# Kernel tuning notes

Measured on AMD Instinct MI355X. Metric: run time of the kernel, lower is better.

The kernel has to match this reference:

```python
import jax, jax.numpy as jnp
import numpy as np
from jax import lax

NUM_HEADS = 8
DIM = 384
B, H, W = 4, 128, 128
NEG_INF = -1e30


def setup_inputs() -> dict:
    key = jax.random.key(0)
    ks = jax.random.split(key, 5)
    x = jax.random.normal(ks[0], (B, DIM, H, W), dtype=jnp.float32)
    qkv_w = jax.random.normal(ks[1], (3 * DIM, DIM), dtype=jnp.float32) * 0.02   # 1x1 conv weight
    dw_w = jax.random.normal(ks[2], (3 * DIM, 1, 3, 3), dtype=jnp.float32) * 0.02  # depthwise 3x3
    proj_w = jax.random.normal(ks[3], (DIM, DIM), dtype=jnp.float32) * 0.02     # 1x1 conv weight
    temperature = jnp.ones((NUM_HEADS, 1, 1), dtype=jnp.float32)
    a1 = jnp.array([0.2], dtype=jnp.float32)
    a2 = jnp.array([0.2], dtype=jnp.float32)
    a3 = jnp.array([0.2], dtype=jnp.float32)
    a4 = jnp.array([0.2], dtype=jnp.float32)
    return {"x": x, "qkv_w": qkv_w, "dw_w": dw_w, "proj_w": proj_w,
            "temperature": temperature, "a1": a1, "a2": a2, "a3": a3, "a4": a4}


def _topk_softmax(attn, k):
    # keep top-k along last dim, softmax over kept entries (threshold == k-th largest)
    thr = lax.top_k(attn, k)[0][..., -1:]
    return jax.nn.softmax(jnp.where(attn >= thr, attn, NEG_INF), axis=-1)


def reference(x, qkv_w, dw_w, proj_w, temperature, a1, a2, a3, a4):
    b, c, h, w = x.shape
    head = NUM_HEADS
    C = c // head          # per-head channel dim (48)
    n = h * w              # token dim

    qkv = jnp.einsum('bchw,oc->bohw', x, qkv_w)  # 1x1 conv, no bias
    qkv = lax.conv_general_dilated(
        qkv, dw_w, window_strides=(1, 1), padding='SAME',
        feature_group_count=3 * c,
        dimension_numbers=('NCHW', 'OIHW', 'NCHW'))  # depthwise 3x3
    q, k, v = jnp.split(qkv, 3, axis=1)

    def heads(t):
        return t.reshape(b, head, C, n)  # b head c (h w)
    q, k, v = heads(q), heads(k), heads(v)

    q = q / jnp.linalg.norm(q, axis=-1, keepdims=True)
    k = k / jnp.linalg.norm(k, axis=-1, keepdims=True)

    attn = jnp.einsum('bhcn,bhdn->bhcd', q, k) * temperature  # [b,head,C,C]

    ks = [int(C / 2), int(C * 2 / 3), int(C * 3 / 4), int(C * 4 / 5)]
    weights = [a1, a2, a3, a4]
    out = jnp.zeros_like(v)
    for kk, a in zip(ks, weights):
        p = _topk_softmax(attn, kk)
        out = out + a * jnp.einsum('bhcd,bhdn->bhcn', p, v)

    out = out.reshape(b, c, h, w)
    out = jnp.einsum('bchw,oc->bohw', out, proj_w)  # 1x1 conv project_out
    return out
```

## Files before the change

### kernel.cpp

```cpp
#include <hip/hip_runtime.h>

#define NHEADS 8
#define DIM 384
#define BB 4
#define HW 16384
#define CPH 48

typedef unsigned int u32;
typedef _Float16 f16x8 __attribute__((ext_vector_type(8)));
typedef _Float16 f16x4 __attribute__((ext_vector_type(4)));
typedef __attribute__((ext_vector_type(4))) float f32x4;

__device__ __forceinline__ float wave_min(float v) {
    #pragma unroll
    for (int off = 32; off; off >>= 1) v = fminf(v, __shfl_xor(v, off));
    return v;
}
__device__ __forceinline__ float wave_max(float v) {
    #pragma unroll
    for (int off = 32; off; off >>= 1) v = fmaxf(v, __shfl_xor(v, off));
    return v;
}
__device__ __forceinline__ float wave_sum(float v) {
    #pragma unroll
    for (int off = 32; off; off >>= 1) v += __shfl_xor(v, off);
    return v;
}

__device__ __forceinline__ u32 pack2h(float a, float b) {
    union { _Float16 h[2]; u32 u; } p;
    p.h[0] = (_Float16)a; p.h[1] = (_Float16)b;
    return p.u;
}

#define GLOBAL_TO_LDS16(gsrc, ldst)                                           \
    __builtin_amdgcn_global_load_lds(                                         \
        (const __attribute__((address_space(1))) u32*)(gsrc),                 \
        (__attribute__((address_space(3))) u32*)(ldst), 16, 0, 0)

__global__ void cvt_w(const float* __restrict__ a, _Float16* __restrict__ o, int n)
{
    const int i = blockIdx.x * 256 + threadIdx.x;
    if (i < n) o[i] = (_Float16)a[i];
}

__global__ __launch_bounds__(256) void transpose_cvt(
    const float* __restrict__ x, _Float16* __restrict__ xt)
{
    const int n0 = blockIdx.x * 64;
    const int c0 = blockIdx.y * 192;
    const int b  = blockIdx.z;
    __shared__ u32 tile[64 * 97];
    const int t = threadIdx.x, w = t >> 6, l = t & 63;

    const float* xb = x + ((size_t)b * DIM + c0) * HW + n0 + l;
    #pragma unroll 4
    for (int j = 0; j < 24; ++j) {
        const int cc = j * 8 + w * 2;
        const float v0 = xb[(size_t)cc * HW];
        const float v1 = xb[(size_t)(cc + 1) * HW];
        tile[l * 97 + (cc >> 1)] = pack2h(v0, v1);
    }
    __syncthreads();

    _Float16* ob = xt + ((size_t)b * HW + n0) * DIM + c0;
    #pragma unroll
    for (int it = 0; it < 6; ++it) {
        const int elem = it * 2048 + t * 8;
        const int nl = elem / 192, col = elem % 192;
        const int base = nl * 97 + (col >> 1);
        u32 out4[4] = { tile[base], tile[base + 1], tile[base + 2], tile[base + 3] };
        *(uint4*)&ob[(size_t)nl * DIM + col] = *(const uint4*)out4;
    }
}

__global__ __launch_bounds__(256) void transpose16(
    const _Float16* __restrict__ in, _Float16* __restrict__ ot)
{
    const int n0 = blockIdx.x * 128;
    const int c0 = blockIdx.y * 192;
    const int b  = blockIdx.z;
    __shared__ _Float16 tile[128 * 194];
    const int t = threadIdx.x, w = t >> 6, l = t & 63;

    const _Float16* ib = in + ((size_t)b * DIM + c0) * HW + n0 + 2 * l;
    #pragma unroll 4
    for (int j = 0; j < 48; ++j) {
        const int cc = j * 4 + w;
        union { u32 u; _Float16 h[2]; } v;
        v.u = *(const u32*)&ib[(size_t)cc * HW];
        tile[(2 * l) * 194 + cc]     = v.h[0];
        tile[(2 * l + 1) * 194 + cc] = v.h[1];
    }
    __syncthreads();

    _Float16* ob = ot + ((size_t)b * HW + n0) * DIM + c0;
    #pragma unroll
    for (int it = 0; it < 12; ++it) {
        const int elem = it * 2048 + t * 8;
        const int nl = elem / 192, col = elem % 192;
        const _Float16* src = &tile[nl * 194 + col];
        u32 out4[4];
        out4[0] = *(const u32*)&src[0];
        out4[1] = *(const u32*)&src[2];
        out4[2] = *(const u32*)&src[4];
        out4[3] = *(const u32*)&src[6];
        *(uint4*)&ob[(size_t)nl * DIM + col] = *(const uint4*)out4;
    }
}

__global__ __launch_bounds__(256) void gemm_f16(
    const _Float16* __restrict__ W, const _Float16* __restrict__ Xt,
    void* __restrict__ Y, int out_f32, int wbs)
{
    const int n0 = blockIdx.x * 128;
    const int m0 = blockIdx.y * 128;
    const int b  = blockIdx.z;

    __shared__ _Float16 sA[128 * 32];
    __shared__ _Float16 sB[128 * 32];

    const int t = threadIdx.x;
    const int w = t >> 6;
    const int l = t & 63;

    const _Float16* gA = W + (size_t)b * wbs
                           + ((size_t)(m0 + w * 32 + (l >> 2))) * DIM + (l & 3) * 8;
    const _Float16* gB = Xt + ((size_t)b * HW + n0 + w * 32 + (l >> 2)) * DIM + (l & 3) * 8;
    _Float16* lA = &sA[(w * 32) * 32];
    _Float16* lB = &sB[(w * 32) * 32];

    f32x4 acc[4][4];
    #pragma unroll
    for (int i = 0; i < 4; ++i)
        #pragma unroll
        for (int j = 0; j < 4; ++j)
            acc[i][j] = (f32x4){0.f, 0.f, 0.f, 0.f};

    const int wm = (w >> 1) * 64, wn = (w & 1) * 64;
    const int fr = l & 15, fk = (l >> 4) * 8;

    for (int k0 = 0; k0 < DIM; k0 += 32) {
        __syncthreads();
        GLOBAL_TO_LDS16(gA + k0,             lA);
        GLOBAL_TO_LDS16(gA + k0 + 16 * DIM,  lA + 16 * 32);
        GLOBAL_TO_LDS16(gB + k0,             lB);
        GLOBAL_TO_LDS16(gB + k0 + 16 * DIM,  lB + 16 * 32);
        __syncthreads();

        f16x8 af[4], bfv[4];
        #pragma unroll
        for (int mi = 0; mi < 4; ++mi)
            af[mi] = *(const f16x8*)&sA[(wm + mi * 16 + fr) * 32 + fk];
        #pragma unroll
        for (int ni = 0; ni < 4; ++ni)
            bfv[ni] = *(const f16x8*)&sB[(wn + ni * 16 + fr) * 32 + fk];
        #pragma unroll
        for (int mi = 0; mi < 4; ++mi)
            #pragma unroll
            for (int ni = 0; ni < 4; ++ni)
                acc[mi][ni] = __builtin_amdgcn_mfma_f32_16x16x32_f16(
                    af[mi], bfv[ni], acc[mi][ni], 0, 0, 0);
    }

    const int er = (l >> 4) * 4;
    if (out_f32) {
        float* Yp = (float*)Y + (size_t)b * DIM * HW;
        #pragma unroll
        for (int mi = 0; mi < 4; ++mi)
            #pragma unroll
            for (int ni = 0; ni < 4; ++ni)
                #pragma unroll
                for (int r = 0; r < 4; ++r)
                    Yp[(size_t)(m0 + wm + mi * 16 + er + r) * HW + n0 + wn + ni * 16 + fr]
                        = acc[mi][ni][r];
    } else {
        _Float16* Yp = (_Float16*)Y + (size_t)b * DIM * HW;
        #pragma unroll
        for (int mi = 0; mi < 4; ++mi)
            #pragma unroll
            for (int ni = 0; ni < 4; ++ni)
                #pragma unroll
                for (int r = 0; r < 4; ++r)
                    Yp[(size_t)(m0 + wm + mi * 16 + er + r) * HW + n0 + wn + ni * 16 + fr]
                        = (_Float16)acc[mi][ni][r];
    }
}

__global__ __launch_bounds__(256) void dwconv_f16(
    const _Float16* __restrict__ in, const float* __restrict__ w9,
    _Float16* __restrict__ out, float* __restrict__ ss, int ss_off)
{
    const int j  = blockIdx.x & 3;
    const int p  = blockIdx.x >> 2;
    const int cl = p % DIM;
    const int b  = p / DIM;
    const int r0 = j * 32;

    __shared__ __align__(16) _Float16 tile[34 * 136 + 8];
    const int t = threadIdx.x;

    const uint4 z4 = make_uint4(0, 0, 0, 0);
    for (int i = t; i < 579; i += 256)
        *(uint4*)&tile[i * 8] = z4;
    __syncthreads();

    const _Float16* ip = in + (size_t)p * HW;
    for (int c = t; c < 34 * 16; c += 256) {
        const int i = c >> 4, seg = c & 15;
        const int g = r0 - 1 + i;
        if ((unsigned)g < 128u)
            *(f16x8*)&tile[i * 136 + 8 + seg * 8] = *(const f16x8*)&ip[g * 128 + seg * 8];
    }

    float w[9];
    #pragma unroll
    for (int i = 0; i < 9; ++i) w[i] = w9[cl * 9 + i];
    __syncthreads();

    const int yr = t >> 3;
    const int xc = (t & 7) * 16;

    float acc[16];
    #pragma unroll
    for (int c = 0; c < 16; ++c) acc[c] = 0.f;

    #pragma unroll
    for (int dy = 0; dy < 3; ++dy) {
        const _Float16* rp = &tile[(yr + dy) * 136 + xc];
        const f16x8 v0 = *(const f16x8*)&rp[0];
        const f16x8 v1 = *(const f16x8*)&rp[8];
        const f16x8 v2 = *(const f16x8*)&rp[16];
        const f16x8 v3 = *(const f16x8*)&rp[24];
        float rv[18];
        #pragma unroll
        for (int i = 0; i < 18; ++i) {
            const int idx = 7 + i;
            const _Float16 h = (idx < 8)  ? v0[idx]
                             : (idx < 16) ? v1[idx - 8]
                             : (idx < 24) ? v2[idx - 16]
                                          : v3[idx - 24];
            rv[i] = (float)h;
        }
        const float w0 = w[dy * 3 + 0], w1 = w[dy * 3 + 1], w2 = w[dy * 3 + 2];
        #pragma unroll
        for (int c = 0; c < 16; ++c) {
            acc[c] = fmaf(rv[c],     w0, acc[c]);
            acc[c] = fmaf(rv[c + 1], w1, acc[c]);
            acc[c] = fmaf(rv[c + 2], w2, acc[c]);
        }
    }

    alignas(16) _Float16 oh[16];
    float ssum = 0.f;
    #pragma unroll
    for (int c = 0; c < 16; ++c) {
        oh[c] = (_Float16)acc[c];
        ssum = fmaf(acc[c], acc[c], ssum);
    }
    _Float16* op = out + (size_t)p * HW + (r0 + yr) * 128 + xc;
    *(f16x8*)&op[0] = *(const f16x8*)&oh[0];
    *(f16x8*)&op[8] = *(const f16x8*)&oh[8];

    if (ss != nullptr) {
        __syncthreads();
        float* red = (float*)tile;
        red[t] = ssum;
        __syncthreads();
        for (int s = 128; s > 0; s >>= 1) {
            if (t < s) red[t] += red[t + s];
            __syncthreads();
        }
        if (t == 0) atomicAdd(&ss[b * (2 * DIM) + ss_off + cl], red[0]);
    }
}

#define GNC 1024
__global__ __launch_bounds__(256) void gram_qk(
    const _Float16* __restrict__ qA, const _Float16* __restrict__ kA,
    float* __restrict__ G)
{
    const int n0 = blockIdx.x * GNC;
    const int h  = blockIdx.y;
    const int b  = blockIdx.z;
    const _Float16* qb = qA + ((size_t)b * DIM + h * CPH) * HW + n0;
    const _Float16* kb = kA + ((size_t)b * DIM + h * CPH) * HW + n0;

    const int t = threadIdx.x;
    const int w = t >> 6, l = t & 63;
    const int fr = l & 15, fk = (l >> 4) * 8;

    f32x4 acc[3][3];
    #pragma unroll
    for (int i = 0; i < 3; ++i)
        #pragma unroll
        for (int j = 0; j < 3; ++j)
            acc[i][j] = (f32x4){0.f, 0.f, 0.f, 0.f};

    const int nbase = w * (GNC / 4);
    #pragma unroll 4
    for (int nn = 0; nn < GNC / 4; nn += 32) {
        f16x8 qf[3], kf[3];
        #pragma unroll
        for (int i = 0; i < 3; ++i) {
            const size_t off = (size_t)(i * 16 + fr) * HW + nbase + nn + fk;
            qf[i] = *(const f16x8*)&qb[off];
            kf[i] = *(const f16x8*)&kb[off];
        }
        #pragma unroll
        for (int i = 0; i < 3; ++i)
            #pragma unroll
            for (int j = 0; j < 3; ++j)
                acc[i][j] = __builtin_amdgcn_mfma_f32_16x16x32_f16(
                    qf[i], kf[j], acc[i][j], 0, 0, 0);
    }

    __shared__ float red[4][CPH * CPH];
    const int er = (l >> 4) * 4;
    #pragma unroll
    for (int i = 0; i < 3; ++i)
        #pragma unroll
        for (int j = 0; j < 3; ++j)
            #pragma unroll
            for (int r = 0; r < 4; ++r)
                red[w][(i * 16 + er + r) * CPH + j * 16 + fr] = acc[i][j][r];
    __syncthreads();

    float* Gp = G + ((size_t)(b * NHEADS + h)) * CPH * CPH;
    for (int i = t; i < CPH * CPH; i += 256)
        atomicAdd(&Gp[i], red[0][i] + red[1][i] + red[2][i] + red[3][i]);
}

__global__ __launch_bounds__(64) void topk_combine(
    const float* __restrict__ G, const float* __restrict__ ss,
    const float* __restrict__ temp,
    const float* __restrict__ a1, const float* __restrict__ a2,
    const float* __restrict__ a3, const float* __restrict__ a4,
    float* __restrict__ P)
{
    const int row = blockIdx.x;
    const int bh  = row / CPH;
    const int r   = row - bh * CPH;
    const int b = bh >> 3, h = bh & 7;
    const int l = threadIdx.x;

    const float tpr = temp[h];
    const float* ssb = ss + b * (2 * DIM);
    const float invq = 1.f / sqrtf(ssb[h * CPH + r]);

    float att = -3.0e38f;
    if (l < CPH)
        att = G[(size_t)row * CPH + l] * invq * (1.f / sqrtf(ssb[DIM + h * CPH + l])) * tpr;

    int cnt = 0;
    #pragma unroll
    for (int i = 0; i < CPH; ++i)
        cnt += (__shfl(att, i) > att) ? 1 : 0;

    const float mx   = wave_max(att);
    const float thr0 = wave_min((l < CPH && cnt < 24) ? att : 3.0e38f);
    const float thr1 = wave_min((l < CPH && cnt < 32) ? att : 3.0e38f);
    const float thr2 = wave_min((l < CPH && cnt < 36) ? att : 3.0e38f);
    const float thr3 = wave_min((l < CPH && cnt < 38) ? att : 3.0e38f);

    const float e = (l < CPH) ? expf(att - mx) : 0.f;
    const float Z0 = wave_sum(att >= thr0 ? e : 0.f);
    const float Z1 = wave_sum(att >= thr1 ? e : 0.f);
    const float Z2 = wave_sum(att >= thr2 ? e : 0.f);
    const float Z3 = wave_sum(att >= thr3 ? e : 0.f);

    const float w0 = a1[0] / Z0, w1 = a2[0] / Z1, w2 = a3[0] / Z2, w3 = a4[0] / Z3;
    float pv = 0.f;
    if (att >= thr0) pv += w0 * e;
    if (att >= thr1) pv += w1 * e;
    if (att >= thr2) pv += w2 * e;
    if (att >= thr3) pv += w3 * e;
    if (l < CPH) P[(size_t)row * CPH + l] = pv;
}

__global__ __launch_bounds__(256) void fuse_pw(
    const float* __restrict__ pw, const float* __restrict__ P,
    _Float16* __restrict__ Wf)
{
    const int o0 = blockIdx.x * CPH;
    const int h  = blockIdx.y;
    const int b  = blockIdx.z;
    const int t  = threadIdx.x;

    __shared__ float sP[CPH][CPH];
    __shared__ float sW[CPH][CPH + 1];
    for (int i = t; i < CPH * CPH; i += 256) {
        const int r = i / CPH, cc = i % CPH;
        sP[r][cc] = P[((size_t)(b * NHEADS + h)) * CPH * CPH + i];
        sW[r][cc] = pw[(size_t)(o0 + r) * DIM + h * CPH + cc];
    }
    __syncthreads();

    for (int i = t; i < CPH * CPH; i += 256) {
        const int o = i / CPH, d = i % CPH;
        float s = 0.f;
        #pragma unroll
        for (int c = 0; c < CPH; ++c)
            s = fmaf(sW[o][c], sP[c][d], s);
        Wf[((size_t)b * DIM + o0 + o) * DIM + h * CPH + d] = (_Float16)s;
    }
}

extern "C" void kernel_launch(void* const* d_in, const int* in_sizes, int n_in,
                              void* d_out, int out_size, void* d_ws, size_t ws_size,
                              hipStream_t stream)
{
    const float* x      = (const float*)d_in[0];
    const float* qkv_w  = (const float*)d_in[1];
    const float* dw_w   = (const float*)d_in[2];
    const float* proj_w = (const float*)d_in[3];
    const float* temp   = (const float*)d_in[4];
    const float* a1 = (const float*)d_in[5];
    const float* a2 = (const float*)d_in[6];
    const float* a3 = (const float*)d_in[7];
    const float* a4 = (const float*)d_in[8];
    float* out = (float*)d_out;

    const size_t PBE = (size_t)HW * DIM;
    const size_t WQE = (size_t)1152 * 384;
    const size_t WPE = (size_t)384 * 384;

    auto need_for = [&](size_t nb) -> size_t {
        return nb * PBE * 2 * 4 + (WQE + nb * WPE) * 2
             + (nb * 768 + 2 * nb * NHEADS * CPH * CPH) * 4;
    };

    int nb, npass;
    if      (ws_size >= need_for(4)) { nb = 4; npass = 1; }
    else if (ws_size >= need_for(2)) { nb = 2; npass = 2; }
    else if (ws_size >= need_for(1)) { nb = 1; npass = 4; }
    else return;

    _Float16* A  = (_Float16*)d_ws;
    _Float16* C  = A + (size_t)nb * PBE;
    _Float16* D  = C + (size_t)nb * PBE;
    _Float16* E  = D + (size_t)nb * PBE;
    _Float16* wq = E + (size_t)nb * PBE;
    _Float16* Wf = wq + WQE;
    float* buf_ss = (float*)(Wf + (size_t)nb * WPE);
    float* buf_G  = buf_ss + (size_t)nb * 768;
    float* buf_P  = buf_G + (size_t)nb * NHEADS * CPH * CPH;

    cvt_w<<<dim3((1152 * 384 + 255) / 256), 256, 0, stream>>>(qkv_w, wq, 1152 * 384);

    for (int p = 0; p < npass; ++p) {
        const int b0 = p * nb;
        const float* xp   = x   + (size_t)b0 * PBE;
        float*       outp = out + (size_t)b0 * PBE;

        const dim3 ggrid(HW / 128, DIM / 128, nb);
        const dim3 dgrid(nb * DIM * 4);

        transpose_cvt<<<dim3(HW / 64, 2, nb), 256, 0, stream>>>(xp, A);
        hipMemsetAsync(buf_ss, 0,
                       ((size_t)nb * 768 + (size_t)nb * NHEADS * CPH * CPH) * sizeof(float),
                       stream);

        gemm_f16<<<ggrid, 256, 0, stream>>>(wq, A, C, 0, 0);
        dwconv_f16<<<dgrid, 256, 0, stream>>>(C, dw_w, D, buf_ss, 0);
        gemm_f16<<<ggrid, 256, 0, stream>>>(wq + (size_t)DIM * DIM, A, C, 0, 0);
        dwconv_f16<<<dgrid, 256, 0, stream>>>(C, dw_w + (size_t)DIM * 9, E, buf_ss, DIM);

        gram_qk<<<dim3(HW / GNC, NHEADS, nb), 256, 0, stream>>>(D, E, buf_G);
        topk_combine<<<dim3(nb * NHEADS * CPH), 64, 0, stream>>>(
            buf_G, buf_ss, temp, a1, a2, a3, a4, buf_P);

        gemm_f16<<<ggrid, 256, 0, stream>>>(wq + (size_t)2 * DIM * DIM, A, C, 0, 0);
        dwconv_f16<<<dgrid, 256, 0, stream>>>(C, dw_w + (size_t)2 * DIM * 9, D, nullptr, 0);

        fuse_pw<<<dim3(DIM / CPH, NHEADS, nb), 256, 0, stream>>>(proj_w, buf_P, Wf);

        transpose16<<<dim3(HW / 128, 2, nb), 256, 0, stream>>>(D, A);

        gemm_f16<<<ggrid, 256, 0, stream>>>(Wf, A, outp, 1, (int)WPE);
    }
}
```

Measured before the change: 472.9 us.

## Merge q/k/v 1x1 conv into one GEMM and one depthwise launch

Replaces three separate 384-row qkv GEMMs and three depthwise-conv launches with one GEMM over all 1152 output channels and one depthwise kernel that routes each channel group to the q, k or v buffer. Only q and k channels accumulate sum-of-squares. This cuts launch count, gives each launch more blocks, and reads the transposed input once per GEMM pass instead of three times. In exchange the workspace grows to hold the full 1152-channel intermediate, which may force smaller batch passes when memory is tight.

```diff
diff --git a/kernel.cpp b/kernel.cpp
--- a/kernel.cpp
+++ b/kernel.cpp
@@ -116,6 +116,7 @@
     const int n0 = blockIdx.x * 128;
     const int m0 = blockIdx.y * 128;
     const int b  = blockIdx.z;
+    const int M  = gridDim.y * 128;
 
     __shared__ _Float16 sA[128 * 32];
     __shared__ _Float16 sB[128 * 32];
@@ -165,7 +166,7 @@
 
     const int er = (l >> 4) * 4;
     if (out_f32) {
-        float* Yp = (float*)Y + (size_t)b * DIM * HW;
+        float* Yp = (float*)Y + (size_t)b * M * HW;
         #pragma unroll
         for (int mi = 0; mi < 4; ++mi)
             #pragma unroll
@@ -175,7 +176,7 @@
                     Yp[(size_t)(m0 + wm + mi * 16 + er + r) * HW + n0 + wn + ni * 16 + fr]
                         = acc[mi][ni][r];
     } else {
-        _Float16* Yp = (_Float16*)Y + (size_t)b * DIM * HW;
+        _Float16* Yp = (_Float16*)Y + (size_t)b * M * HW;
         #pragma unroll
         for (int mi = 0; mi < 4; ++mi)
             #pragma unroll
@@ -187,14 +188,15 @@
     }
 }
 
-__global__ __launch_bounds__(256) void dwconv_f16(
+__global__ __launch_bounds__(256) void dwconv_all(
     const _Float16* __restrict__ in, const float* __restrict__ w9,
-    _Float16* __restrict__ out, float* __restrict__ ss, int ss_off)
+    _Float16* __restrict__ oq, _Float16* __restrict__ ok_,
+    _Float16* __restrict__ ov, float* __restrict__ ss)
 {
     const int j  = blockIdx.x & 3;
     const int p  = blockIdx.x >> 2;
-    const int cl = p % DIM;
-    const int b  = p / DIM;
+    const int c  = p % 1152;
+    const int b  = p / 1152;
     const int r0 = j * 32;
 
     __shared__ __align__(16) _Float16 tile[34 * 136 + 8];
@@ -206,8 +208,8 @@
     __syncthreads();
 
     const _Float16* ip = in + (size_t)p * HW;
-    for (int c = t; c < 34 * 16; c += 256) {
-        const int i = c >> 4, seg = c & 15;
+    for (int cc = t; cc < 34 * 16; cc += 256) {
+        const int i = cc >> 4, seg = cc & 15;
         const int g = r0 - 1 + i;
         if ((unsigned)g < 128u)
             *(f16x8*)&tile[i * 136 + 8 + seg * 8] = *(const f16x8*)&ip[g * 128 + seg * 8];
@@ -215,7 +217,7 @@
 
     float w[9];
     #pragma unroll
-    for (int i = 0; i < 9; ++i) w[i] = w9[cl * 9 + i];
+    for (int i = 0; i < 9; ++i) w[i] = w9[c * 9 + i];
     __syncthreads();
 
     const int yr = t >> 3;
@@ -223,7 +225,7 @@
 
     float acc[16];
     #pragma unroll
-    for (int c = 0; c < 16; ++c) acc[c] = 0.f;
+    for (int cc = 0; cc < 16; ++cc) acc[cc] = 0.f;
 
     #pragma unroll
     for (int dy = 0; dy < 3; ++dy) {
@@ -244,25 +246,28 @@
         }
         const float w0 = w[dy * 3 + 0], w1 = w[dy * 3 + 1], w2 = w[dy * 3 + 2];
         #pragma unroll
-        for (int c = 0; c < 16; ++c) {
-            acc[c] = fmaf(rv[c],     w0, acc[c]);
-            acc[c] = fmaf(rv[c + 1], w1, acc[c]);
-            acc[c] = fmaf(rv[c + 2], w2, acc[c]);
+        for (int cc = 0; cc < 16; ++cc) {
+            acc[cc] = fmaf(rv[cc],     w0, acc[cc]);
+            acc[cc] = fmaf(rv[cc + 1], w1, acc[cc]);
+            acc[cc] = fmaf(rv[cc + 2], w2, acc[cc]);
         }
     }
 
     alignas(16) _Float16 oh[16];
     float ssum = 0.f;
     #pragma unroll
-    for (int c = 0; c < 16; ++c) {
-        oh[c] = (_Float16)acc[c];
-        ssum = fmaf(acc[c], acc[c], ssum);
-    }
-    _Float16* op = out + (size_t)p * HW + (r0 + yr) * 128 + xc;
+    for (int cc = 0; cc < 16; ++cc) {
+        oh[cc] = (_Float16)acc[cc];
+        ssum = fmaf(acc[cc], acc[cc], ssum);
+    }
+    const int grp = c / 384;
+    const int cl  = c - grp * 384;
+    _Float16* obase = (grp == 0) ? oq : (grp == 1) ? ok_ : ov;
+    _Float16* op = obase + ((size_t)b * DIM + cl) * HW + (r0 + yr) * 128 + xc;
     *(f16x8*)&op[0] = *(const f16x8*)&oh[0];
     *(f16x8*)&op[8] = *(const f16x8*)&oh[8];
 
-    if (ss != nullptr) {
+    if (c < 768) {
         __syncthreads();
         float* red = (float*)tile;
         red[t] = ssum;
@@ -271,7 +276,7 @@
             if (t < s) red[t] += red[t + s];
             __syncthreads();
         }
-        if (t == 0) atomicAdd(&ss[b * (2 * DIM) + ss_off + cl], red[0]);
+        if (t == 0) atomicAdd(&ss[b * (2 * DIM) + c], red[0]);
     }
 }
 
@@ -426,7 +431,7 @@
     const size_t WPE = (size_t)384 * 384;
 
     auto need_for = [&](size_t nb) -> size_t {
-        return nb * PBE * 2 * 4 + (WQE + nb * WPE) * 2
+        return nb * PBE * 2 * 7 + (WQE + nb * WPE) * 2
              + (nb * 768 + 2 * nb * NHEADS * CPH * CPH) * 4;
     };
 
@@ -438,9 +443,10 @@
 
     _Float16* A  = (_Float16*)d_ws;
     _Float16* C  = A + (size_t)nb * PBE;
-    _Float16* D  = C + (size_t)nb * PBE;
+    _Float16* D  = C + (size_t)3 * nb * PBE;
     _Float16* E  = D + (size_t)nb * PBE;
-    _Float16* wq = E + (size_t)nb * PBE;
+    _Float16* F  = E + (size_t)nb * PBE;
+    _Float16* wq = F + (size_t)nb * PBE;
     _Float16* Wf = wq + WQE;
     float* buf_ss = (float*)(Wf + (size_t)nb * WPE);
     float* buf_G  = buf_ss + (size_t)nb * 768;
@@ -453,30 +459,23 @@
         const float* xp   = x   + (size_t)b0 * PBE;
         float*       outp = out + (size_t)b0 * PBE;
 
-        const dim3 ggrid(HW / 128, DIM / 128, nb);
-        const dim3 dgrid(nb * DIM * 4);
-
         transpose_cvt<<<dim3(HW / 64, 2, nb), 256, 0, stream>>>(xp, A);
         hipMemsetAsync(buf_ss, 0,
                        ((size_t)nb * 768 + (size_t)nb * NHEADS * CPH * CPH) * sizeof(float),
                        stream);
 
-        gemm_f16<<<ggrid, 256, 0, stream>>>(wq, A, C, 0, 0);
-        dwconv_f16<<<dgrid, 256, 0, stream>>>(C, dw_w, D, buf_ss, 0);
-        gemm_f16<<<ggrid, 256, 0, stream>>>(wq + (size_t)DIM * DIM, A, C, 0, 0);
-        dwconv_f16<<<dgrid, 256, 0, stream>>>(C, dw_w + (size_t)DIM * 9, E, buf_ss, DIM);
+        gemm_f16<<<dim3(HW / 128, 1152 / 128, nb), 256, 0, stream>>>(wq, A, C, 0, 0);
+
+        dwconv_all<<<dim3(nb * 1152 * 4), 256, 0, stream>>>(C, dw_w, D, E, F, buf_ss);
 
         gram_qk<<<dim3(HW / GNC, NHEADS, nb), 256, 0, stream>>>(D, E, buf_G);
         topk_combine<<<dim3(nb * NHEADS * CPH), 64, 0, stream>>>(
             buf_G, buf_ss, temp, a1, a2, a3, a4, buf_P);
 
-        gemm_f16<<<ggrid, 256, 0, stream>>>(wq + (size_t)2 * DIM * DIM, A, C, 0, 0);
-        dwconv_f16<<<dgrid, 256, 0, stream>>>(C, dw_w + (size_t)2 * DIM * 9, D, nullptr, 0);
-
         fuse_pw<<<dim3(DIM / CPH, NHEADS, nb), 256, 0, stream>>>(proj_w, buf_P, Wf);
 
-        transpose16<<<dim3(HW / 128, 2, nb), 256, 0, stream>>>(D, A);
-
-        gemm_f16<<<ggrid, 256, 0, stream>>>(Wf, A, outp, 1, (int)WPE);
-    }
-}
+        transpose16<<<dim3(HW / 128, 2, nb), 256, 0, stream>>>(F, A);
+
+        gemm_f16<<<dim3(HW / 128, DIM / 128, nb), 256, 0, stream>>>(Wf, A, outp, 1, (int)WPE);
+    }
+}
```

Result: faster. 459.3 us (-2.9%).
